# Optimization experiments

Measured on AMD Instinct MI355X. Metric: run time of the kernel, lower is better.

The kernel has to match this reference:

```python
import jax, jax.numpy as jnp
import numpy as np


def _rnn_scan(x_pre, W_hh, b_hh, h0):
    # x_pre: [S, B, H] precomputed input projection; returns stacked h: [S, B, H]
    def step(h, xp):
        h = jnp.tanh(xp + h @ W_hh.T + b_hh)
        return h, h
    _, hs = jax.lax.scan(step, h0, x_pre)
    return hs


def setup_inputs() -> dict:
    key = jax.random.key(0)
    ks = jax.random.split(key, 12)
    B, S, E, H, V = 16, 256, 512, 1024, 32000
    sE, sH = 1.0 / np.sqrt(E), 1.0 / np.sqrt(H)
    return {
        "x_ids": jax.random.randint(ks[0], (B, S), 0, V),
        "emb": jax.random.normal(ks[1], (V, E), jnp.float32),
        "W_ih1": jax.random.normal(ks[2], (H, E), jnp.float32) * sE,
        "b_ih1": jax.random.normal(ks[3], (H,), jnp.float32) * sH,
        "W_hh1": jax.random.normal(ks[4], (H, H), jnp.float32) * sH,
        "b_hh1": jax.random.normal(ks[5], (H,), jnp.float32) * sH,
        "W_ih2": jax.random.normal(ks[6], (H, H), jnp.float32) * sH,
        "b_ih2": jax.random.normal(ks[7], (H,), jnp.float32) * sH,
        "W_hh2": jax.random.normal(ks[8], (H, H), jnp.float32) * sH,
        "b_hh2": jax.random.normal(ks[9], (H,), jnp.float32) * sH,
        "W_fc": jax.random.normal(ks[10], (V, H), jnp.float32) * sH,
        "b_fc": jax.random.normal(ks[11], (V,), jnp.float32) * sH,
    }


def reference(x_ids, emb, W_ih1, b_ih1, W_hh1, b_hh1, W_ih2, b_ih2, W_hh2, b_hh2, W_fc, b_fc):
    B, S = x_ids.shape
    H = W_hh1.shape[0]
    x = emb[x_ids]  # [B, S, E]
    # layer 1: precompute input projection for all steps, scan over time
    x1 = jnp.einsum('bse,he->sbh', x, W_ih1) + b_ih1  # [S, B, H]
    h0 = jnp.zeros((B, H), x.dtype)
    h1s = _rnn_scan(x1, W_hh1, b_hh1, h0)  # [S, B, H]
    # layer 2
    x2 = jnp.einsum('sbh,gh->sbg', h1s, W_ih2) + b_ih2
    h2s = _rnn_scan(x2, W_hh2, b_hh2, h0)  # [S, B, H]
    # per-step fc + softmax, vectorized
    logits = jnp.einsum('sbh,vh->bsv', h2s, W_fc) + b_fc  # [B, S, V]
    return jax.nn.softmax(logits, axis=-1)
```

## Files before the change

### kernel.cpp

```cpp
#include <hip/hip_runtime.h>
#include <cstdint>
#include <cstddef>

typedef unsigned short u16;
typedef __attribute__((ext_vector_type(4))) float f32x4;
typedef __attribute__((ext_vector_type(8))) short s16x8;
typedef __attribute__((ext_vector_type(8))) unsigned short u16x8;
typedef __attribute__((ext_vector_type(4))) unsigned short u16x4;
typedef __attribute__((ext_vector_type(4))) unsigned u32x4;

#define B_ 16
#define S_ 256
#define E_ 512
#define H_ 1024
#define V_ 32000
#define M_TOK (S_*B_)
#define BH (B_*H_)
#define NT_FC 250
#define MT_FC 32
#define NSM  (M_TOK/4)

__device__ __forceinline__ u16 f2bf(float f) {
  union { float f; unsigned u; } x; x.f = f;
  unsigned r = x.u + 0x7fffu + ((x.u >> 16) & 1u);
  return (u16)(r >> 16);
}
__device__ __forceinline__ float bf2f(u16 x) {
  union { unsigned u; float f; } c; c.u = ((unsigned)x) << 16; return c.f;
}

__device__ __forceinline__ void sc_load16(s16x8& d, const u16* p) {
  asm volatile("global_load_dwordx4 %0, %1, off sc0 sc1" : "=v"(d) : "v"(p));
}
__device__ __forceinline__ void sc_load16u(u32x4& d, const u16* p) {
  asm volatile("global_load_dwordx4 %0, %1, off sc0 sc1" : "=v"(d) : "v"(p));
}
__device__ __forceinline__ void sc_load8w(u16x4& d, const u16* p) {
  asm volatile("global_load_dwordx2 %0, %1, off sc0 sc1\n\ts_waitcnt vmcnt(0)"
               : "=v"(d) : "v"(p) : "memory");
}
__device__ __forceinline__ int sc_load4w(const int* p) {
  int d;
  asm volatile("global_load_dword %0, %1, off sc0 sc1\n\ts_waitcnt vmcnt(0)"
               : "=v"(d) : "v"(p) : "memory");
  return d;
}
__device__ __forceinline__ void sc_store8(u16* p, u16x4 v) {
  asm volatile("global_store_dwordx2 %0, %1, off sc0 sc1" :: "v"(p), "v"(v) : "memory");
}
__device__ __forceinline__ void sc_store4(int* p, int v) {
  asm volatile("global_store_dword %0, %1, off sc0 sc1" :: "v"(p), "v"(v) : "memory");
}
__device__ __forceinline__ void sc_store4f(float* p, float v) {
  asm volatile("global_store_dword %0, %1, off sc0 sc1" :: "v"(p), "v"(v) : "memory");
}
__device__ __forceinline__ void wait_vm0() {
  asm volatile("s_waitcnt vmcnt(0)" ::: "memory");
}

__global__ __launch_bounds__(256)
void k_cvt_all(const float* s0, u16* d0, int n0,
               const float* s1, u16* d1, int n1,
               const float* s2, u16* d2, int n2,
               const float* s3, u16* d3, int n3,
               const float* s4, u16* d4, int n4)
{
  const int total = n0 + n1 + n2 + n3 + n4;
  for (int i = blockIdx.x*256 + threadIdx.x; i < total; i += gridDim.x*256) {
    const float* s; u16* d; int j = i;
    if (j < n0) { s = s0; d = d0; }
    else { j -= n0;
      if (j < n1) { s = s1; d = d1; }
      else { j -= n1;
        if (j < n2) { s = s2; d = d2; }
        else { j -= n2;
          if (j < n3) { s = s3; d = d3; }
          else { j -= n3; s = s4; d = d4; } } } }
    float4 v = reinterpret_cast<const float4*>(s)[j];
    ushort4 o;
    o.x = f2bf(v.x); o.y = f2bf(v.y); o.z = f2bf(v.z); o.w = f2bf(v.w);
    reinterpret_cast<ushort4*>(d)[j] = o;
  }
}

__global__ __launch_bounds__(256) void k_embed(const int* __restrict__ ids,
                                               const float* __restrict__ emb,
                                               u16* __restrict__ A1) {
  int g = blockIdx.x*256 + threadIdx.x;
  int m = g >> 6;
  int c = g & 63;
  int s = m >> 4, b = m & 15;
  int id = ids[b*S_ + s];
  const float4* src = reinterpret_cast<const float4*>(emb + (size_t)id*E_ + (size_t)c*8);
  float4 v0 = src[0], v1 = src[1];
  u16x8 o;
  o[0]=f2bf(v0.x); o[1]=f2bf(v0.y); o[2]=f2bf(v0.z); o[3]=f2bf(v0.w);
  o[4]=f2bf(v1.x); o[5]=f2bf(v1.y); o[6]=f2bf(v1.z); o[7]=f2bf(v1.w);
  *reinterpret_cast<u16x8*>(A1 + (size_t)m*E_ + (size_t)c*8) = o;
}

#define BM 128
#define BN 128
#define BK 32

__device__ __forceinline__ void gload_lds16(const u16* g, u16* l) {
  __builtin_amdgcn_global_load_lds(
      (const __attribute__((address_space(1))) void*)g,
      (__attribute__((address_space(3))) void*)l,
      16, 0, 0);
}

template<int FCMODE>
__global__ __launch_bounds__(256)
void k_gemm(const u16* __restrict__ A, const u16* __restrict__ Bw,
            float* __restrict__ C, const float* __restrict__ bias,
            int M, int N, int K)
{
  __shared__ u16 lA[2][BM*BK];
  __shared__ u16 lB[2][BN*BK];
  const int tid = threadIdx.x;
  const int l = tid & 63, w = tid >> 6;

  const int nwg = gridDim.x * gridDim.y;
  int d = blockIdx.y * gridDim.x + blockIdx.x;
  int tt = (d & 7) * (nwg >> 3) + (d >> 3);
  const int n0 = (tt / gridDim.y) * BN;
  const int m0 = (tt % gridDim.y) * BM;

  const int wr = w >> 1, wc = w & 1;

  const int L0 = (w*2+0)*64 + l;
  const int L1 = (w*2+1)*64 + l;
  const int r0 = L0 >> 2, r1 = L1 >> 2;
  const int c0 = (L0 & 3) ^ ((r0 >> 1) & 3);
  const int c1 = (L1 & 3) ^ ((r1 >> 1) & 3);
  const u16* gA0 = A  + (size_t)(m0 + r0)*K + c0*8;
  const u16* gA1 = A  + (size_t)(m0 + r1)*K + c1*8;
  const u16* gB0 = Bw + (size_t)(n0 + r0)*K + c0*8;
  const u16* gB1 = Bw + (size_t)(n0 + r1)*K + c1*8;

  const int fr = l & 15;
  const int xc = (l >> 4) ^ ((fr >> 1) & 3);
  int aoff[4], boff[4];
#pragma unroll
  for (int f = 0; f < 4; ++f) {
    aoff[f] = (wr*64 + f*16 + fr) * BK + xc*8;
    boff[f] = (wc*64 + f*16 + fr) * BK + xc*8;
  }

  f32x4 acc[4][4] = {};
  const int KT = K / BK;

  gload_lds16(gA0, &lA[0][(w*2+0)*512]);
  gload_lds16(gA1, &lA[0][(w*2+1)*512]);
  gload_lds16(gB0, &lB[0][(w*2+0)*512]);
  gload_lds16(gB1, &lB[0][(w*2+1)*512]);
  __syncthreads();

  for (int kt = 0; kt < KT; ++kt) {
    const int buf = kt & 1;
    if (kt + 1 < KT) {
      const int koff = (kt+1)*BK;
      gload_lds16(gA0 + koff, &lA[buf^1][(w*2+0)*512]);
      gload_lds16(gA1 + koff, &lA[buf^1][(w*2+1)*512]);
      gload_lds16(gB0 + koff, &lB[buf^1][(w*2+0)*512]);
      gload_lds16(gB1 + koff, &lB[buf^1][(w*2+1)*512]);
    }
    s16x8 af[4], bq[4];
#pragma unroll
    for (int f = 0; f < 4; ++f) af[f] = *reinterpret_cast<const s16x8*>(&lA[buf][aoff[f]]);
#pragma unroll
    for (int f = 0; f < 4; ++f) bq[f] = *reinterpret_cast<const s16x8*>(&lB[buf][boff[f]]);
#pragma unroll
    for (int fm = 0; fm < 4; ++fm)
#pragma unroll
      for (int fn = 0; fn < 4; ++fn)
        acc[fm][fn] = __builtin_amdgcn_mfma_f32_16x16x32_bf16(af[fm], bq[fn], acc[fm][fn], 0, 0, 0);
    __syncthreads();
  }

  const int rowb = (l >> 4) * 4;
  const int colb = l & 15;
#pragma unroll
  for (int fm = 0; fm < 4; ++fm) {
#pragma unroll
    for (int fn = 0; fn < 4; ++fn) {
      const int col = n0 + wc*64 + fn*16 + colb;
#pragma unroll
      for (int r = 0; r < 4; ++r) {
        const int row = m0 + wr*64 + fm*16 + rowb + r;
        float v = acc[fm][fn][r];
        if (FCMODE == 2) {
          ((u16*)C)[(size_t)row*N + col] = f2bf(v);
        } else {
          C[(size_t)row*N + col] = v;
        }
      }
    }
  }
}

__device__ __forceinline__ void fc_tile(const u16* __restrict__ A, const u16* __restrict__ Bw,
                                        float* __restrict__ C, const float* __restrict__ bias,
                                        int m0, int n0, u16* smem, int scmode)
{
  const int tid = threadIdx.x;
  const int l = tid & 63, w = tid >> 6;
  const int wr = w >> 1, wc = w & 1;
  u16* lA = smem;
  u16* lB = smem + 8192;

  const int L0 = (w*2+0)*64 + l;
  const int L1 = (w*2+1)*64 + l;
  const int r0 = L0 >> 2, r1 = L1 >> 2;
  const int c0 = (L0 & 3) ^ ((r0 >> 1) & 3);
  const int c1 = (L1 & 3) ^ ((r1 >> 1) & 3);
  const u16* gA0 = A  + (size_t)(m0 + r0)*H_ + c0*8;
  const u16* gA1 = A  + (size_t)(m0 + r1)*H_ + c1*8;
  const u16* gB0 = Bw + (size_t)(n0 + r0)*H_ + c0*8;
  const u16* gB1 = Bw + (size_t)(n0 + r1)*H_ + c1*8;

  const int fr = l & 15;
  const int xc = (l >> 4) ^ ((fr >> 1) & 3);
  int aoff[4], boff[4];
#pragma unroll
  for (int f = 0; f < 4; ++f) {
    aoff[f] = (wr*64 + f*16 + fr) * BK + xc*8;
    boff[f] = (wc*64 + f*16 + fr) * BK + xc*8;
  }

  f32x4 acc[4][4] = {};

  gload_lds16(gA0, lA + (w*2+0)*512);
  gload_lds16(gA1, lA + (w*2+1)*512);
  gload_lds16(gB0, lB + (w*2+0)*512);
  gload_lds16(gB1, lB + (w*2+1)*512);
  __syncthreads();

  for (int kt = 0; kt < 32; ++kt) {
    const int buf = kt & 1;
    if (kt + 1 < 32) {
      const int koff = (kt+1)*BK;
      gload_lds16(gA0 + koff, lA + (buf^1)*4096 + (w*2+0)*512);
      gload_lds16(gA1 + koff, lA + (buf^1)*4096 + (w*2+1)*512);
      gload_lds16(gB0 + koff, lB + (buf^1)*4096 + (w*2+0)*512);
      gload_lds16(gB1 + koff, lB + (buf^1)*4096 + (w*2+1)*512);
    }
    s16x8 af[4], bq[4];
#pragma unroll
    for (int f = 0; f < 4; ++f) af[f] = *reinterpret_cast<const s16x8*>(lA + buf*4096 + aoff[f]);
#pragma unroll
    for (int f = 0; f < 4; ++f) bq[f] = *reinterpret_cast<const s16x8*>(lB + buf*4096 + boff[f]);
#pragma unroll
    for (int fm = 0; fm < 4; ++fm)
#pragma unroll
      for (int fn = 0; fn < 4; ++fn)
        acc[fm][fn] = __builtin_amdgcn_mfma_f32_16x16x32_bf16(af[fm], bq[fn], acc[fm][fn], 0, 0, 0);
    __syncthreads();
  }

  const int rowb = (l >> 4) * 4;
  const int colb = l & 15;
#pragma unroll
  for (int fm = 0; fm < 4; ++fm) {
#pragma unroll
    for (int fn = 0; fn < 4; ++fn) {
      const int col = n0 + wc*64 + fn*16 + colb;
      const float bv = bias[col];
#pragma unroll
      for (int r = 0; r < 4; ++r) {
        const int row = m0 + wr*64 + fm*16 + rowb + r;
        const int b = row & 15, s = row >> 4;
        float* p = C + ((size_t)(b*S_ + s))*V_ + col;
        float v = acc[fm][fn][r] + bv;
        if (scmode) sc_store4f(p, v);
        else        *p = v;
      }
    }
  }
}

__device__ __forceinline__ void softmax_row(float* row, int l) {
  float m = -3.4e38f, s = 0.f;
  for (int it = 0; it < 125; ++it) {
    float4 v = reinterpret_cast<const float4*>(row)[it*64 + l];
    float cm = fmaxf(fmaxf(v.x, v.y), fmaxf(v.z, v.w));
    float nm = fmaxf(m, cm);
    s = s*__expf(m - nm) + __expf(v.x-nm) + __expf(v.y-nm) + __expf(v.z-nm) + __expf(v.w-nm);
    m = nm;
  }
#pragma unroll
  for (int o = 32; o; o >>= 1) {
    float m2 = __shfl_xor(m, o), s2 = __shfl_xor(s, o);
    float nm = fmaxf(m, m2);
    s = s*__expf(m - nm) + s2*__expf(m2 - nm);
    m = nm;
  }
  const float inv = 1.f / s;
  for (int it = 0; it < 125; ++it) {
    float4 v = reinterpret_cast<const float4*>(row)[it*64 + l];
    float4 p;
    p.x = __expf(v.x - m)*inv; p.y = __expf(v.y - m)*inv;
    p.z = __expf(v.z - m)*inv; p.w = __expf(v.w - m)*inv;
    reinterpret_cast<float4*>(row)[it*64 + l] = p;
  }
}

__global__ __launch_bounds__(256)
void k_mega(const u16* __restrict__ Whh1, const u16* __restrict__ Wih2,
            const u16* __restrict__ Whh2, const u16* __restrict__ x1b,
            const float* __restrict__ bih1, const float* __restrict__ bhh1,
            const float* __restrict__ bih2, const float* __restrict__ bhh2,
            u16* __restrict__ h1s, u16* __restrict__ u2s, u16* __restrict__ h2s,
            int* __restrict__ s1, int* __restrict__ su, int* __restrict__ s2,
            const u16* __restrict__ Wfcb, const float* __restrict__ bfc,
            float* __restrict__ out, int* __restrict__ prog2,
            int* __restrict__ done, int* __restrict__ fcdone, int* __restrict__ smdone)
{
  __shared__ u16 smem[16384];
  const int bid = blockIdx.x;
  const int tid = threadIdx.x;

  if (bid < 48) {
    const int l = tid & 63, w = tid >> 6;
    const int role = bid >> 4;
    const int blk  = bid & 15;
    const int rowA = blk*64 + w*16 + (l & 15);
    const int kc = l >> 4;
    const int bcol = l & 15;
    const int i0 = blk*64 + w*16 + kc*4;
    const int jme = (tid & 127) >> 3;

    const u16* Wsel = (role == 0) ? Whh1 : (role == 1) ? Wih2 : Whh2;
    s16x8 wf[32];
    {
      const u16* wp = Wsel + (size_t)rowA*H_ + kc*8;
#pragma unroll
      for (int ks = 0; ks < 32; ++ks) wf[ks] = *reinterpret_cast<const s16x8*>(wp + ks*32);
    }

    auto stage = [&](const u16* src, const int* sentrow) {
      while (sc_load4w(sentrow + jme) != 0) __builtin_amdgcn_s_sleep(2);
      s16x8 stg[8];
#pragma unroll
      for (int r = 0; r < 8; ++r) sc_load16(stg[r], src + (size_t)(tid + r*256)*8);
      wait_vm0();
#pragma unroll
      for (int r = 0; r < 8; ++r) {
        int idx8 = tid + r*256;
        int bt = idx8 >> 7, c8 = idx8 & 127;
        *reinterpret_cast<s16x8*>(reinterpret_cast<char*>(smem) +
            bt*2048 + ((c8*16) ^ ((bt & 7) << 4))) = stg[r];
      }
    };

    const int swz = (bcol & 7) << 4;
    auto hfrag = [&](int ks) -> s16x8 {
      return *reinterpret_cast<const s16x8*>(
          reinterpret_cast<const char*>(smem) + bcol*2048 + (((kc*16) + ks*64) ^ swz));
    };
    auto mfma32 = [&](f32x4& a0, f32x4& a1, f32x4& a2, f32x4& a3) {
#pragma unroll
      for (int ks = 0; ks < 32; ks += 4) {
        a0 = __builtin_amdgcn_mfma_f32_16x16x32_bf16(wf[ks+0], hfrag(ks+0), a0, 0, 0, 0);
        a1 = __builtin_amdgcn_mfma_f32_16x16x32_bf16(wf[ks+1], hfrag(ks+1), a1, 0, 0, 0);
        a2 = __builtin_amdgcn_mfma_f32_16x16x32_bf16(wf[ks+2], hfrag(ks+2), a2, 0, 0, 0);
        a3 = __builtin_amdgcn_mfma_f32_16x16x32_bf16(wf[ks+3], hfrag(ks+3), a3, 0, 0, 0);
      }
    };

    if (role == 0) {
      float bc[4];
#pragma unroll
      for (int r = 0; r < 4; ++r) bc[r] = bih1[i0+r] + bhh1[i0+r];
      for (int t = 0; t < S_; ++t) {
        f32x4 a0 = {}, a1 = {}, a2 = {}, a3 = {};
        if (t > 0) {
          stage(h1s + (size_t)(t-1)*BH, s1 + (t-1)*16);
          __syncthreads();
          mfma32(a0, a1, a2, a3);
        }
        u16x4 xr = *reinterpret_cast<const u16x4*>(x1b + (size_t)(t*B_ + bcol)*H_ + i0);
        f32x4 tot = (a0 + a1) + (a2 + a3);
        u16x4 o;
        o[0] = f2bf(tanhf(tot[0] + bf2f(xr[0]) + bc[0]));
        o[1] = f2bf(tanhf(tot[1] + bf2f(xr[1]) + bc[1]));
        o[2] = f2bf(tanhf(tot[2] + bf2f(xr[2]) + bc[2]));
        o[3] = f2bf(tanhf(tot[3] + bf2f(xr[3]) + bc[3]));
        sc_store8(h1s + (size_t)(t*B_ + bcol)*H_ + i0, o);
        wait_vm0();
        __syncthreads();
        if (tid == 0) sc_store4(s1 + t*16 + blk, 0);
      }
    } else if (role == 1) {
      float bc[4];
#pragma unroll
      for (int r = 0; r < 4; ++r) bc[r] = bih2[i0+r] + bhh2[i0+r];
      for (int t = 0; t < S_; ++t) {
        stage(h1s + (size_t)t*BH, s1 + t*16);
        __syncthreads();
        f32x4 a0 = {}, a1 = {}, a2 = {}, a3 = {};
        mfma32(a0, a1, a2, a3);
        f32x4 tot = (a0 + a1) + (a2 + a3);
        u16x4 o;
        o[0] = f2bf(tot[0] + bc[0]);
        o[1] = f2bf(tot[1] + bc[1]);
        o[2] = f2bf(tot[2] + bc[2]);
        o[3] = f2bf(tot[3] + bc[3]);
        sc_store8(u2s + (size_t)(t*B_ + bcol)*H_ + i0, o);
        wait_vm0();
        __syncthreads();
        if (tid == 0) sc_store4(su + t*16 + blk, 0);
      }
    } else {
      for (int t = 0; t < S_; ++t) {
        if (tid == 0) {
          while (sc_load4w(su + t*16 + blk) != 0) __builtin_amdgcn_s_sleep(2);
        }
        if (t > 0) stage(h2s + (size_t)(t-1)*BH, s2 + (t-1)*16);
        __syncthreads();
        u16x4 uv;
        sc_load8w(uv, u2s + (size_t)(t*B_ + bcol)*H_ + i0);
        f32x4 a0 = {}, a1 = {}, a2 = {}, a3 = {};
        if (t > 0) mfma32(a0, a1, a2, a3);
        f32x4 tot = (a0 + a1) + (a2 + a3);
        u16x4 o;
        o[0] = f2bf(tanhf(tot[0] + bf2f(uv[0])));
        o[1] = f2bf(tanhf(tot[1] + bf2f(uv[1])));
        o[2] = f2bf(tanhf(tot[2] + bf2f(uv[2])));
        o[3] = f2bf(tanhf(tot[3] + bf2f(uv[3])));
        sc_store8(h2s + (size_t)(t*B_ + bcol)*H_ + i0, o);
        wait_vm0();
        __syncthreads();
        if (tid == 0) {
          sc_store4(s2 + t*16 + blk, 0);
          sc_store4(prog2 + blk, t + 1);
        }
      }
    }
    return;
  }

  if (bid < 48 + MT_FC*NT_FC) {
    const int q = bid - 48;
    const int mt = q / NT_FC;
    const int nt = q - mt * NT_FC;
    const unsigned need = (unsigned)((mt + 1) * 8);

    __shared__ int s_ok;
    if (tid == 0) {
      int ok = 0;
      const u16* pp = (const u16*)prog2;
      for (int it = 0; it < 2500; ++it) {
        u32x4 pa, pb, pc, pd;
        sc_load16u(pa, pp); sc_load16u(pb, pp + 8);
        sc_load16u(pc, pp + 16); sc_load16u(pd, pp + 24);
        wait_vm0();
        unsigned m0 = pa[0] < pa[1] ? pa[0] : pa[1];
        unsigned m1 = pa[2] < pa[3] ? pa[2] : pa[3];
        unsigned m2 = pb[0] < pb[1] ? pb[0] : pb[1];
        unsigned m3 = pb[2] < pb[3] ? pb[2] : pb[3];
        unsigned m4 = pc[0] < pc[1] ? pc[0] : pc[1];
        unsigned m5 = pc[2] < pc[3] ? pc[2] : pc[3];
        unsigned m6 = pd[0] < pd[1] ? pd[0] : pd[1];
        unsigned m7 = pd[2] < pd[3] ? pd[2] : pd[3];
        m0 = m0 < m1 ? m0 : m1;  m2 = m2 < m3 ? m2 : m3;
        m4 = m4 < m5 ? m4 : m5;  m6 = m6 < m7 ? m6 : m7;
        m0 = m0 < m2 ? m0 : m2;  m4 = m4 < m6 ? m4 : m6;
        unsigned mn = m0 < m4 ? m0 : m4;
        if (mn >= need) { ok = 1; break; }
        __builtin_amdgcn_s_sleep(32);
      }
      s_ok = ok;
    }
    __syncthreads();
    if (!s_ok) return;

    fc_tile(h2s, Wfcb, out, bfc, mt*BM, nt*BN, smem, 1);
    wait_vm0();
    __syncthreads();
    if (tid == 0) {
      done[q] = 1;
      __hip_atomic_fetch_add(fcdone + mt, 1, __ATOMIC_RELAXED, __HIP_MEMORY_SCOPE_AGENT);
    }
    return;
  }

  const int sq = bid - 48 - MT_FC*NT_FC;
  if (sq >= NSM) return;
  const int mt = sq >> 5;

  __shared__ int s_ok2;
  if (tid == 0) {
    int ok = 0;
    for (int it = 0; it < 4000; ++it) {
      if (sc_load4w(fcdone + mt) >= NT_FC) { ok = 1; break; }
      __builtin_amdgcn_s_sleep(32);
    }
    s_ok2 = ok;
  }
  __syncthreads();
  if (!s_ok2) return;

  const int wv = tid >> 6, l = tid & 63;
  const int m = sq*4 + wv;
  const int b = m & 15, s = m >> 4;
  softmax_row(out + ((size_t)b*S_ + s)*V_, l);
  __syncthreads();
  if (tid == 0) smdone[sq] = 1;
}

__global__ __launch_bounds__(256)
void k_fc_cleanup(const u16* __restrict__ h2s, const u16* __restrict__ Wfcb,
                  const float* __restrict__ bfc, float* __restrict__ out,
                  const int* __restrict__ done)
{
  __shared__ u16 smem[16384];
  const int q = blockIdx.x;
  if (done[q]) return;
  const int mt = q / NT_FC;
  const int nt = q - mt * NT_FC;
  fc_tile(h2s, Wfcb, out, bfc, mt*BM, nt*BN, smem, 0);
}

__global__ __launch_bounds__(256)
void k_softmax_cleanup(float* __restrict__ out, const int* __restrict__ smdone) {
  const int sq = blockIdx.x;
  if (smdone[sq]) return;
  const int wv = threadIdx.x >> 6, l = threadIdx.x & 63;
  const int m = sq*4 + wv;
  const int b = m & 15, s = m >> 4;
  softmax_row(out + ((size_t)b*S_ + s)*V_, l);
}

extern "C" void kernel_launch(void* const* d_in, const int* in_sizes, int n_in,
                              void* d_out, int out_size, void* d_ws, size_t ws_size,
                              hipStream_t stream) {
  (void)in_sizes; (void)n_in; (void)out_size; (void)ws_size;
  const int*   x_ids = (const int*)  d_in[0];
  const float* emb   = (const float*)d_in[1];
  const float* Wih1  = (const float*)d_in[2];
  const float* bih1  = (const float*)d_in[3];
  const float* Whh1  = (const float*)d_in[4];
  const float* bhh1  = (const float*)d_in[5];
  const float* Wih2  = (const float*)d_in[6];
  const float* bih2  = (const float*)d_in[7];
  const float* Whh2  = (const float*)d_in[8];
  const float* bhh2  = (const float*)d_in[9];
  const float* Wfc   = (const float*)d_in[10];
  const float* bfc   = (const float*)d_in[11];
  float* out = (float*)d_out;

  char* ws = (char*)d_ws;
  size_t off = 0;
  auto alloc = [&](size_t bytes) {
    char* p = ws + off; off += (bytes + 255) & ~(size_t)255; return p;
  };
  int* sent   = (int*) alloc(3 * S_ * 16 * 4);
  const int CTRL_INTS = 16 + MT_FC*NT_FC + 32 + NSM;
  int* ctrl   = (int*) alloc(CTRL_INTS * 4);
  u16* Wfcb   = (u16*) alloc((size_t)V_*H_*2);
  u16* Whh1b  = (u16*) alloc((size_t)H_*H_*2);
  u16* Wih2b  = (u16*) alloc((size_t)H_*H_*2);
  u16* Whh2b  = (u16*) alloc((size_t)H_*H_*2);
  u16* x1b    = (u16*) alloc((size_t)M_TOK*H_*2);
  u16* h1s    = (u16*) alloc((size_t)M_TOK*H_*2);
  u16* u2s    = (u16*) alloc((size_t)M_TOK*H_*2);
  u16* h2s    = (u16*) alloc((size_t)M_TOK*H_*2);
  u16* A1     = (u16*) alloc((size_t)M_TOK*E_*2);
  u16* Wih1b  = (u16*) alloc((size_t)H_*E_*2);
  int* s1 = sent, *su = sent + S_*16, *s2 = sent + 2*S_*16;
  int* prog2  = ctrl;
  int* done   = ctrl + 16;
  int* fcdone = done + MT_FC*NT_FC;
  int* smdone = fcdone + 32;

  k_cvt_all<<<2048, 256, 0, stream>>>(Wih1, Wih1b, H_*E_/4,
                                      Whh1, Whh1b, H_*H_/4,
                                      Wih2, Wih2b, H_*H_/4,
                                      Whh2, Whh2b, H_*H_/4,
                                      Wfc,  Wfcb,  V_*H_/4);
  k_embed<<<M_TOK*64/256, 256, 0, stream>>>(x_ids, emb, A1);

  k_gemm<2><<<dim3(H_/BN, M_TOK/BM), 256, 0, stream>>>(A1, Wih1b, (float*)x1b, nullptr, M_TOK, H_, E_);

  hipMemsetAsync(sent, 0xFF, 3 * S_ * 16 * 4, stream);
  hipMemsetAsync(ctrl, 0, CTRL_INTS * 4, stream);

  k_mega<<<48 + MT_FC*NT_FC + NSM, 256, 0, stream>>>(
      Whh1b, Wih2b, Whh2b, x1b, bih1, bhh1, bih2, bhh2,
      h1s, u2s, h2s, s1, su, s2, Wfcb, bfc, out, prog2, done, fcdone, smdone);

  k_fc_cleanup<<<MT_FC*NT_FC, 256, 0, stream>>>(h2s, Wfcb, bfc, out, done);
  k_softmax_cleanup<<<NSM, 256, 0, stream>>>(out, smdone);
}
```

Before: 1.723 ms.

## Fuse softmax partial sums into FC epilogue and interleave norm blocks per row tile

The FC tile epilogue now computes per-row sums of exp(logit) for its 128 columns and writes them to a stats buffer, so the softmax pass only sums 250 partials and does one read-exp-write pass instead of two passes over each row. Normalization blocks are also interleaved with the FC blocks of the same row tile in the grid ordering, so they schedule right after their producers. This drops the max subtraction, which relies on logits being small enough that exp cannot overflow. It also adds a stats buffer and an extra shared-memory reduction with a barrier in every FC tile.

```diff
diff --git a/kernel.cpp b/kernel.cpp
--- a/kernel.cpp
+++ b/kernel.cpp
@@ -1,6 +1,7 @@
 #include <hip/hip_runtime.h>
 #include <cstdint>
 #include <cstddef>
+#include <math.h>
 
 typedef unsigned short u16;
 typedef __attribute__((ext_vector_type(4))) float f32x4;
@@ -18,7 +19,7 @@
 #define BH (B_*H_)
 #define NT_FC 250
 #define MT_FC 32
-#define NSM  (M_TOK/4)
+#define GRP (NT_FC+32)
 
 __device__ __forceinline__ u16 f2bf(float f) {
   union { float f; unsigned u; } x; x.f = f;
@@ -53,6 +54,9 @@
 }
 __device__ __forceinline__ void sc_store4f(float* p, float v) {
   asm volatile("global_store_dword %0, %1, off sc0 sc1" :: "v"(p), "v"(v) : "memory");
+}
+__device__ __forceinline__ void sc_store16f(float* p, f32x4 v) {
+  asm volatile("global_store_dwordx4 %0, %1, off sc0 sc1" :: "v"(p), "v"(v) : "memory");
 }
 __device__ __forceinline__ void wait_vm0() {
   asm volatile("s_waitcnt vmcnt(0)" ::: "memory");
@@ -200,13 +204,16 @@
   }
 }
 
+template<int SC>
 __device__ __forceinline__ void fc_tile(const u16* __restrict__ A, const u16* __restrict__ Bw,
                                         float* __restrict__ C, const float* __restrict__ bias,
-                                        int m0, int n0, u16* smem, int scmode)
+                                        float* __restrict__ stat,
+                                        int m0, int n0, u16* smem)
 {
   const int tid = threadIdx.x;
   const int l = tid & 63, w = tid >> 6;
   const int wr = w >> 1, wc = w & 1;
+  const int nt = n0 / BN;
   u16* lA = smem;
   u16* lB = smem + 8192;
 
@@ -261,6 +268,7 @@
 
   const int rowb = (l >> 4) * 4;
   const int colb = l & 15;
+
 #pragma unroll
   for (int fm = 0; fm < 4; ++fm) {
 #pragma unroll
@@ -271,38 +279,51 @@
       for (int r = 0; r < 4; ++r) {
         const int row = m0 + wr*64 + fm*16 + rowb + r;
         const int b = row & 15, s = row >> 4;
+        acc[fm][fn][r] += bv;
         float* p = C + ((size_t)(b*S_ + s))*V_ + col;
-        float v = acc[fm][fn][r] + bv;
-        if (scmode) sc_store4f(p, v);
-        else        *p = v;
-      }
-    }
-  }
-}
-
-__device__ __forceinline__ void softmax_row(float* row, int l) {
-  float m = -3.4e38f, s = 0.f;
+        if (SC) sc_store4f(p, acc[fm][fn][r]);
+        else    *p = acc[fm][fn][r];
+      }
+    }
+  }
+
+  float* stats = reinterpret_cast<float*>(smem);
+#pragma unroll
+  for (int fm = 0; fm < 4; ++fm) {
+#pragma unroll
+    for (int r = 0; r < 4; ++r) {
+      float sm = __expf(acc[fm][0][r]) + __expf(acc[fm][1][r])
+               + __expf(acc[fm][2][r]) + __expf(acc[fm][3][r]);
+#pragma unroll
+      for (int o = 1; o <= 8; o <<= 1) sm += __shfl_xor(sm, o);
+      if (colb == 0) {
+        const int j = wr*64 + fm*16 + rowb + r;
+        stats[j*2 + wc] = sm;
+      }
+    }
+  }
+  __syncthreads();
+  if (tid < 128) {
+    float sm = stats[tid*2 + 0] + stats[tid*2 + 1];
+    float* p = stat + (size_t)(m0 + tid)*NT_FC + nt;
+    if (SC) sc_store4f(p, sm);
+    else    *p = sm;
+  }
+}
+
+__device__ __forceinline__ void norm_row(float* __restrict__ row,
+                                         const float* __restrict__ strow, int l) {
+  float sum = 0.f;
+  for (int i = l; i < NT_FC; i += 64) sum += strow[i];
+#pragma unroll
+  for (int o = 32; o; o >>= 1) sum += __shfl_xor(sum, o);
+  const float inv = 1.f / sum;
   for (int it = 0; it < 125; ++it) {
-    float4 v = reinterpret_cast<const float4*>(row)[it*64 + l];
-    float cm = fmaxf(fmaxf(v.x, v.y), fmaxf(v.z, v.w));
-    float nm = fmaxf(m, cm);
-    s = s*__expf(m - nm) + __expf(v.x-nm) + __expf(v.y-nm) + __expf(v.z-nm) + __expf(v.w-nm);
-    m = nm;
-  }
-#pragma unroll
-  for (int o = 32; o; o >>= 1) {
-    float m2 = __shfl_xor(m, o), s2 = __shfl_xor(s, o);
-    float nm = fmaxf(m, m2);
-    s = s*__expf(m - nm) + s2*__expf(m2 - nm);
-    m = nm;
-  }
-  const float inv = 1.f / s;
-  for (int it = 0; it < 125; ++it) {
-    float4 v = reinterpret_cast<const float4*>(row)[it*64 + l];
-    float4 p;
-    p.x = __expf(v.x - m)*inv; p.y = __expf(v.y - m)*inv;
-    p.z = __expf(v.z - m)*inv; p.w = __expf(v.w - m)*inv;
-    reinterpret_cast<float4*>(row)[it*64 + l] = p;
+    float4 x = reinterpret_cast<const float4*>(row)[it*64 + l];
+    f32x4 p;
+    p[0] = __expf(x.x)*inv; p[1] = __expf(x.y)*inv;
+    p[2] = __expf(x.z)*inv; p[3] = __expf(x.w)*inv;
+    sc_store16f(&row[(it*64 + l)*4], p);
   }
 }
 
@@ -314,8 +335,9 @@
             u16* __restrict__ h1s, u16* __restrict__ u2s, u16* __restrict__ h2s,
             int* __restrict__ s1, int* __restrict__ su, int* __restrict__ s2,
             const u16* __restrict__ Wfcb, const float* __restrict__ bfc,
-            float* __restrict__ out, int* __restrict__ prog2,
-            int* __restrict__ done, int* __restrict__ fcdone, int* __restrict__ smdone)
+            float* __restrict__ out, float* __restrict__ stat,
+            int* __restrict__ prog2, int* __restrict__ done,
+            int* __restrict__ fcdone, int* __restrict__ normdone)
 {
   __shared__ u16 smem[16384];
   const int bid = blockIdx.x;
@@ -441,10 +463,13 @@
     return;
   }
 
-  if (bid < 48 + MT_FC*NT_FC) {
-    const int q = bid - 48;
-    const int mt = q / NT_FC;
-    const int nt = q - mt * NT_FC;
+  const int g = bid - 48;
+  const int mt = g / GRP;
+  const int r  = g - mt * GRP;
+  if (mt >= MT_FC) return;
+
+  if (r < NT_FC) {
+    const int nt = r;
     const unsigned need = (unsigned)((mt + 1) * 8);
 
     __shared__ int s_ok;
@@ -476,20 +501,17 @@
     __syncthreads();
     if (!s_ok) return;
 
-    fc_tile(h2s, Wfcb, out, bfc, mt*BM, nt*BN, smem, 1);
+    fc_tile<1>(h2s, Wfcb, out, bfc, stat, mt*BM, nt*BN, smem);
     wait_vm0();
     __syncthreads();
     if (tid == 0) {
-      done[q] = 1;
+      done[mt*NT_FC + nt] = 1;
       __hip_atomic_fetch_add(fcdone + mt, 1, __ATOMIC_RELAXED, __HIP_MEMORY_SCOPE_AGENT);
     }
     return;
   }
 
-  const int sq = bid - 48 - MT_FC*NT_FC;
-  if (sq >= NSM) return;
-  const int mt = sq >> 5;
-
+  const int chunk = r - NT_FC;
   __shared__ int s_ok2;
   if (tid == 0) {
     int ok = 0;
@@ -503,34 +525,50 @@
   if (!s_ok2) return;
 
   const int wv = tid >> 6, l = tid & 63;
-  const int m = sq*4 + wv;
+  const int m = mt*128 + chunk*4 + wv;
   const int b = m & 15, s = m >> 4;
-  softmax_row(out + ((size_t)b*S_ + s)*V_, l);
+  norm_row(out + ((size_t)b*S_ + s)*V_, stat + (size_t)m*NT_FC, l);
+  wait_vm0();
   __syncthreads();
-  if (tid == 0) smdone[sq] = 1;
+  if (tid == 0) normdone[mt*32 + chunk] = 1;
 }
 
 __global__ __launch_bounds__(256)
 void k_fc_cleanup(const u16* __restrict__ h2s, const u16* __restrict__ Wfcb,
                   const float* __restrict__ bfc, float* __restrict__ out,
-                  const int* __restrict__ done)
+                  float* __restrict__ stat, const int* __restrict__ done)
 {
   __shared__ u16 smem[16384];
   const int q = blockIdx.x;
   if (done[q]) return;
   const int mt = q / NT_FC;
   const int nt = q - mt * NT_FC;
-  fc_tile(h2s, Wfcb, out, bfc, mt*BM, nt*BN, smem, 0);
+  fc_tile<0>(h2s, Wfcb, out, bfc, stat, mt*BM, nt*BN, smem);
 }
 
 __global__ __launch_bounds__(256)
-void k_softmax_cleanup(float* __restrict__ out, const int* __restrict__ smdone) {
+void k_norm_cleanup(float* __restrict__ out, const float* __restrict__ stat,
+                    const int* __restrict__ normdone)
+{
   const int sq = blockIdx.x;
-  if (smdone[sq]) return;
+  if (normdone[sq]) return;
   const int wv = threadIdx.x >> 6, l = threadIdx.x & 63;
   const int m = sq*4 + wv;
   const int b = m & 15, s = m >> 4;
-  softmax_row(out + ((size_t)b*S_ + s)*V_, l);
+  float* row = out + ((size_t)b*S_ + s)*V_;
+  const float* st = stat + (size_t)m*NT_FC;
+  float sum = 0.f;
+  for (int i = l; i < NT_FC; i += 64) sum += st[i];
+#pragma unroll
+  for (int o = 32; o; o >>= 1) sum += __shfl_xor(sum, o);
+  const float inv = 1.f / sum;
+  for (int it = 0; it < 125; ++it) {
+    float4 x = reinterpret_cast<const float4*>(row)[it*64 + l];
+    float4 p;
+    p.x = __expf(x.x)*inv; p.y = __expf(x.y)*inv;
+    p.z = __expf(x.z)*inv; p.w = __expf(x.w)*inv;
+    reinterpret_cast<float4*>(row)[it*64 + l] = p;
+  }
 }
 
 extern "C" void kernel_launch(void* const* d_in, const int* in_sizes, int n_in,
@@ -557,8 +595,9 @@
     char* p = ws + off; off += (bytes + 255) & ~(size_t)255; return p;
   };
   int* sent   = (int*) alloc(3 * S_ * 16 * 4);
-  const int CTRL_INTS = 16 + MT_FC*NT_FC + 32 + NSM;
+  const int CTRL_INTS = 16 + MT_FC*NT_FC + 32 + 1024;
   int* ctrl   = (int*) alloc(CTRL_INTS * 4);
+  float* stat = (float*)alloc((size_t)M_TOK * NT_FC * 4);
   u16* Wfcb   = (u16*) alloc((size_t)V_*H_*2);
   u16* Whh1b  = (u16*) alloc((size_t)H_*H_*2);
   u16* Wih2b  = (u16*) alloc((size_t)H_*H_*2);
@@ -570,10 +609,10 @@
   u16* A1     = (u16*) alloc((size_t)M_TOK*E_*2);
   u16* Wih1b  = (u16*) alloc((size_t)H_*E_*2);
   int* s1 = sent, *su = sent + S_*16, *s2 = sent + 2*S_*16;
-  int* prog2  = ctrl;
-  int* done   = ctrl + 16;
-  int* fcdone = done + MT_FC*NT_FC;
-  int* smdone = fcdone + 32;
+  int* prog2    = ctrl;
+  int* done     = ctrl + 16;
+  int* fcdone   = done + MT_FC*NT_FC;
+  int* normdone = fcdone + 32;
 
   k_cvt_all<<<2048, 256, 0, stream>>>(Wih1, Wih1b, H_*E_/4,
                                       Whh1, Whh1b, H_*H_/4,
@@ -587,10 +626,10 @@
   hipMemsetAsync(sent, 0xFF, 3 * S_ * 16 * 4, stream);
   hipMemsetAsync(ctrl, 0, CTRL_INTS * 4, stream);
 
-  k_mega<<<48 + MT_FC*NT_FC + NSM, 256, 0, stream>>>(
+  k_mega<<<48 + MT_FC*GRP, 256, 0, stream>>>(
       Whh1b, Wih2b, Whh2b, x1b, bih1, bhh1, bih2, bhh2,
-      h1s, u2s, h2s, s1, su, s2, Wfcb, bfc, out, prog2, done, fcdone, smdone);
-
-  k_fc_cleanup<<<MT_FC*NT_FC, 256, 0, stream>>>(h2s, Wfcb, bfc, out, done);
-  k_softmax_cleanup<<<NSM, 256, 0, stream>>>(out, smdone);
-}
+      h1s, u2s, h2s, s1, su, s2, Wfcb, bfc, out, stat, prog2, done, fcdone, normdone);
+
+  k_fc_cleanup<<<MT_FC*NT_FC, 256, 0, stream>>>(h2s, Wfcb, bfc, out, stat, done);
+  k_norm_cleanup<<<1024, 256, 0, stream>>>(out, stat, normdone);
+}
```

Measured after the change: 1.722 ms. Within noise of the previous version (-0.0%).
